# Performance work log

Hardware: AMD Instinct MI355X
Metric: run time of the kernel (lower is better)

Reference implementation:

```python
import jax, jax.numpy as jnp
import numpy as np

N_NODES = 100000
HIDDEN = 64
IN_CH = 128
N_EDGES = 1600000


def setup_inputs() -> dict:
    key = jax.random.key(0)
    ks = jax.random.split(key, 12)
    x = jax.random.normal(ks[0], (N_NODES, IN_CH), dtype=jnp.float32)
    edge_index = jax.random.randint(ks[1], (2, N_EDGES), 0, N_NODES, dtype=jnp.int64)

    def glorot(k, fan_in, fan_out):
        s = jnp.sqrt(6.0 / (fan_in + fan_out)).astype(jnp.float32)
        return jax.random.uniform(k, (fan_in, fan_out), jnp.float32, -s, s)

    return {
        "x": x,
        "edge_index": edge_index,
        # GCNConv layer 1: linear (no bias) + post-aggregation bias
        "W1": glorot(ks[2], IN_CH, HIDDEN),
        "b1": jnp.zeros((HIDDEN,), jnp.float32),
        # GCNConv layer 2
        "W2": glorot(ks[3], HIDDEN, HIDDEN),
        "b2": jnp.zeros((HIDDEN,), jnp.float32),
        # edge classifier MLP: Linear(2H,H) -> ReLU -> Linear(H,2)
        "Wc1": glorot(ks[4], 2 * HIDDEN, HIDDEN),
        "bc1": jnp.zeros((HIDDEN,), jnp.float32),
        "Wc2": glorot(ks[5], HIDDEN, 2),
        "bc2": jnp.zeros((2,), jnp.float32),
    }


def _gcn_forward(x, edge_index, W1, b1, W2, b2, Wc1, bc1, Wc2, bc2):
    n = x.shape[0]
    src, dst = edge_index[0], edge_index[1]
    # add self-loops (PyG GCNConv default)
    loop = jnp.arange(n, dtype=edge_index.dtype)
    a_src = jnp.concatenate([src, loop])  # [E+N]
    a_dst = jnp.concatenate([dst, loop])
    # symmetric normalization: deg over destination with unit edge weights
    deg = jax.ops.segment_sum(jnp.ones(a_dst.shape[0], x.dtype), a_dst, num_segments=n)
    dis = jax.lax.rsqrt(deg)  # deg >= 1 due to self-loops
    norm = dis[a_src] * dis[a_dst]  # [E+N]

    def conv(h, W, b):
        h = h @ W  # [N, H]
        msg = h[a_src] * norm[:, None]  # [E+N, H] gather + scale
        return jax.ops.segment_sum(msg, a_dst, num_segments=n) + b

    h = jax.nn.relu(conv(x, W1, b1))  # dropout is identity in eval mode
    h = conv(h, W2, b2)
    # edge classifier on concatenated endpoint embeddings
    e = jnp.concatenate([h[src], h[dst]], axis=1)  # [E, 2H]
    z = jax.nn.relu(e @ Wc1 + bc1)
    return z @ Wc2 + bc2  # [E, 2]


def reference(x, edge_index, W1, b1, W2, b2, Wc1, bc1, Wc2, bc2):
    return _gcn_forward(x, edge_index, W1, b1, W2, b2, Wc1, bc1, Wc2, bc2)
```

## Files before the change

### kernel.cpp

```cpp
#include <hip/hip_runtime.h>
#include <hip/hip_fp16.h>

#define HID 64

typedef _Float16 half8 __attribute__((ext_vector_type(8)));
typedef _Float16 half4 __attribute__((ext_vector_type(4)));
typedef float f32x4 __attribute__((ext_vector_type(4)));

__global__ void k_count_rank(const int* __restrict__ dst, int* __restrict__ deg,
                             int* __restrict__ rank, int E) {
  int e = blockIdx.x * blockDim.x + threadIdx.x;
  if (e < E) rank[e] = atomicAdd(&deg[dst[e]], 1);
}

__global__ void k_scan1(const int* __restrict__ deg, int* __restrict__ scanout,
                        int* __restrict__ blocksums, float* __restrict__ dis, int n) {
  __shared__ int sdata[256];
  int tid = threadIdx.x;
  int base = blockIdx.x * 1024 + tid * 4;
  int v0 = 0, v1 = 0, v2 = 0, v3 = 0;
  if (base + 0 < n) v0 = deg[base + 0];
  if (base + 1 < n) v1 = deg[base + 1];
  if (base + 2 < n) v2 = deg[base + 2];
  if (base + 3 < n) v3 = deg[base + 3];
  if (base + 0 < n) dis[base + 0] = rsqrtf((float)v0 + 1.0f);
  if (base + 1 < n) dis[base + 1] = rsqrtf((float)v1 + 1.0f);
  if (base + 2 < n) dis[base + 2] = rsqrtf((float)v2 + 1.0f);
  if (base + 3 < n) dis[base + 3] = rsqrtf((float)v3 + 1.0f);
  int tsum = v0 + v1 + v2 + v3;
  sdata[tid] = tsum;
  __syncthreads();
  for (int off = 1; off < 256; off <<= 1) {
    int t = (tid >= off) ? sdata[tid - off] : 0;
    __syncthreads();
    sdata[tid] += t;
    __syncthreads();
  }
  int excl = sdata[tid] - tsum;
  if (base + 0 < n) scanout[base + 0] = excl;
  if (base + 1 < n) scanout[base + 1] = excl + v0;
  if (base + 2 < n) scanout[base + 2] = excl + v0 + v1;
  if (base + 3 < n) scanout[base + 3] = excl + v0 + v1 + v2;
  if (tid == 255) blocksums[blockIdx.x] = sdata[255];
}

__global__ void k_scan2(int* blocksums, int nb) {
  __shared__ int s[128];
  int tid = threadIdx.x;
  int v = (tid < nb) ? blocksums[tid] : 0;
  s[tid] = v;
  __syncthreads();
  for (int off = 1; off < 128; off <<= 1) {
    int t = (tid >= off) ? s[tid - off] : 0;
    __syncthreads();
    s[tid] += t;
    __syncthreads();
  }
  if (tid < nb) blocksums[tid] = s[tid] - v;
}

__global__ void k_scan3(const int* __restrict__ scanout,
                        const int* __restrict__ blocksums, int* __restrict__ rowoff,
                        int n) {
  int i = blockIdx.x * blockDim.x + threadIdx.x;
  if (i < n) rowoff[i] = scanout[i] + blocksums[i >> 10];
}

__global__ void k_scatter_det(const int* __restrict__ src, const int* __restrict__ dst,
                              const int* __restrict__ rowoff,
                              const int* __restrict__ rank,
                              int* __restrict__ csr_src, int E) {
  int e = blockIdx.x * blockDim.x + threadIdx.x;
  if (e >= E) return;
  int pos = rowoff[dst[e]] + rank[e];
  csr_src[pos] = src[e];
}

__global__ void k_pack_all(const float* __restrict__ W1, const float* __restrict__ W2,
                           const float* __restrict__ Wc1, const float* __restrict__ bc1,
                           __half* __restrict__ packW1, __half* __restrict__ packW2,
                           __half* __restrict__ packUV, float* __restrict__ biasUV,
                           __half* __restrict__ ysent) {
  int b = blockIdx.x, tid = threadIdx.x;
  if (b < 4) {
    int t = b * 256 + tid;
    int f = t >> 6, L = t & 63;
    int kc = f >> 2, nb = f & 3;
    int k = 32 * kc + ((L >> 4) << 3);
    int n = (L & 15) + 16 * nb;
    for (int j = 0; j < 8; ++j)
      packW1[(t << 3) + j] = __float2half(W1[(k + j) * 64 + n]);
  } else if (b < 6) {
    int t = (b - 4) * 256 + tid;
    int f = t >> 6, L = t & 63;
    int kc = f >> 2, nb = f & 3;
    int k = 32 * kc + ((L >> 4) << 3);
    int n = (L & 15) + 16 * nb;
    for (int j = 0; j < 8; ++j)
      packW2[(t << 3) + j] = __float2half(W2[(k + j) * 64 + n]);
  } else if (b < 10) {
    int t = (b - 6) * 256 + tid;
    int f = t >> 6, L = t & 63;
    int kc = f >> 3, nb = f & 7;
    int k = 32 * kc + ((L >> 4) << 3);
    int n = (L & 15) + 16 * nb;
    for (int j = 0; j < 8; ++j) {
      float w = (n < 64) ? Wc1[(k + j) * 64 + n] : Wc1[(64 + k + j) * 64 + (n - 64)];
      packUV[(t << 3) + j] = __float2half(w);
    }
  } else {
    if (tid < 128) biasUV[tid] = (tid < 64) ? bc1[tid] : 0.f;
    else if (tid < 192) ysent[tid - 128] = __float2half(0.f);
  }
}

template <int K, int NOUT, bool F32IN>
__global__ __launch_bounds__(256) void k_lin_mfma(
    const void* __restrict__ Xv, const __half* __restrict__ packB,
    const float* __restrict__ bias, const float* __restrict__ dis,
    __half* __restrict__ Y, int n) {
  int wid = blockIdx.x * 4 + (threadIdx.x >> 6);
  int rowbase = wid * 16;
  if (rowbase >= n) return;
  int L = threadIdx.x & 63;
  int m16 = L & 15, quad = L >> 4;
  constexpr int KC = K / 32;
  constexpr int NB = NOUT / 16;

  half8 Bf[KC * NB];
  const half8* packv = (const half8*)packB;
#pragma unroll
  for (int f = 0; f < KC * NB; ++f) Bf[f] = packv[f * 64 + L];

  int r = min(rowbase + m16, n - 1);
  half8 Af[KC];
  if (F32IN) {
    const float* xr = (const float*)Xv + (long)r * K;
#pragma unroll
    for (int kc = 0; kc < KC; ++kc) {
      const float4* xp = (const float4*)(xr + kc * 32 + quad * 8);
      float4 a = xp[0], b = xp[1];
      half8 v = {(_Float16)a.x, (_Float16)a.y, (_Float16)a.z, (_Float16)a.w,
                 (_Float16)b.x, (_Float16)b.y, (_Float16)b.z, (_Float16)b.w};
      Af[kc] = v;
    }
  } else {
    const half8* xr = (const half8*)((const __half*)Xv + (long)r * K);
#pragma unroll
    for (int kc = 0; kc < KC; ++kc) Af[kc] = xr[kc * 4 + quad];
  }

  f32x4 acc[NB];
#pragma unroll
  for (int nb = 0; nb < NB; ++nb) acc[nb] = {0.f, 0.f, 0.f, 0.f};
#pragma unroll
  for (int kc = 0; kc < KC; ++kc)
#pragma unroll
    for (int nb = 0; nb < NB; ++nb)
      acc[nb] = __builtin_amdgcn_mfma_f32_16x16x32_f16(Af[kc], Bf[kc * NB + nb],
                                                       acc[nb], 0, 0, 0);

  float dv[4];
#pragma unroll
  for (int j = 0; j < 4; ++j) {
    int ro = rowbase + quad * 4 + j;
    dv[j] = (dis && ro < n) ? dis[ro] : 1.f;
  }
#pragma unroll
  for (int nb = 0; nb < NB; ++nb) {
    int col = m16 + 16 * nb;
    float bv = bias ? bias[col] : 0.f;
#pragma unroll
    for (int j = 0; j < 4; ++j) {
      int ro = rowbase + quad * 4 + j;
      if (ro < n) {
        float v = (acc[nb][j] + bv) * dv[j];
        Y[(long)ro * NOUT + col] = __float2half(v);
      }
    }
  }
}

__global__ __launch_bounds__(256) void k_agg_csr(
    const __half* __restrict__ Yh, const float* __restrict__ dis,
    const int* __restrict__ rowoff, const int* __restrict__ csr_src,
    const float* __restrict__ b, __half* __restrict__ A, int n, int E, int relu) {
  int node = blockIdx.x * 4 + (threadIdx.x >> 6);
  if (node >= n) return;
  int L = threadIdx.x & 63;
  int sub = L >> 4;
  int cq = L & 15;
  const half4* Y4 = (const half4*)Yh;
  float dd = dis[node];
  int i0 = rowoff[node];
  int end = (node == n - 1) ? E : rowoff[node + 1];

  float z[4][4] = {{0.f}};
  if (sub == 0) {
    half4 hv = Y4[(long)node * 16 + cq];
#pragma unroll
    for (int j = 0; j < 4; ++j) z[0][j] = (float)hv[j];
  }

  int last = end - 1;
  for (int base = i0; base < end; base += 16) {
    int sidx[4];
#pragma unroll
    for (int slot = 0; slot < 4; ++slot) {
      int idx = base + slot * 4 + sub;
      int sl = csr_src[min(idx, last)];
      sidx[slot] = (idx < end) ? sl : n;
    }
#pragma unroll
    for (int slot = 0; slot < 4; ++slot) {
      half4 hv = Y4[(long)sidx[slot] * 16 + cq];
#pragma unroll
      for (int j = 0; j < 4; ++j) z[slot][j] += (float)hv[j];
    }
  }

  float a[4];
#pragma unroll
  for (int j = 0; j < 4; ++j) {
    a[j] = (z[0][j] + z[1][j]) + (z[2][j] + z[3][j]);
    a[j] += __shfl_xor(a[j], 16, 64);
    a[j] += __shfl_xor(a[j], 32, 64);
  }
  if (sub == 0) {
    float4 bb = ((const float4*)b)[cq];
    float v0 = fmaf(a[0], dd, bb.x), v1 = fmaf(a[1], dd, bb.y);
    float v2 = fmaf(a[2], dd, bb.z), v3 = fmaf(a[3], dd, bb.w);
    if (relu) {
      v0 = fmaxf(v0, 0.f); v1 = fmaxf(v1, 0.f);
      v2 = fmaxf(v2, 0.f); v3 = fmaxf(v3, 0.f);
    }
    half4 o = {(_Float16)v0, (_Float16)v1, (_Float16)v2, (_Float16)v3};
    ((half4*)A)[(long)node * 16 + cq] = o;
  }
}

__global__ __launch_bounds__(256) void k_edge_mlp(
    const __half* __restrict__ UV, const int* __restrict__ src,
    const int* __restrict__ dst, const float* __restrict__ Wc2,
    const float* __restrict__ bc2, float* __restrict__ out, int E, int nwaves) {
  int wid = blockIdx.x * 4 + (threadIdx.x >> 6);
  int L = threadIdx.x & 63;
  int sub = L >> 4;
  int cq = L & 15;

  float w0[4], w1[4];
#pragma unroll
  for (int j = 0; j < 4; ++j) {
    int c = cq * 4 + j;
    w0[j] = Wc2[2 * c];
    w1[j] = Wc2[2 * c + 1];
  }
  float ob0 = bc2[0], ob1 = bc2[1];

  const half4* UV4 = (const half4*)UV;
  int last = E - 1;

  for (long base = (long)wid * 32; base < E; base += (long)nwaves * 32) {
    int se[8], de[8];
#pragma unroll
    for (int slot = 0; slot < 8; ++slot) {
      int e = (int)base + slot * 4 + sub;
      int ec = min(e, last);
      se[slot] = src[ec];
      de[slot] = dst[ec];
    }
    half4 uu[8], vv[8];
#pragma unroll
    for (int slot = 0; slot < 8; ++slot) {
      uu[slot] = UV4[(long)se[slot] * 32 + cq];
      vv[slot] = UV4[(long)de[slot] * 32 + 16 + cq];
    }
#pragma unroll
    for (int slot = 0; slot < 8; ++slot) {
      float o0 = 0.f, o1 = 0.f;
#pragma unroll
      for (int j = 0; j < 4; ++j) {
        float v = fmaxf((float)uu[slot][j] + (float)vv[slot][j], 0.f);
        o0 = fmaf(v, w0[j], o0);
        o1 = fmaf(v, w1[j], o1);
      }
      o0 += __shfl_xor(o0, 1, 64);
      o1 += __shfl_xor(o1, 1, 64);
      o0 += __shfl_xor(o0, 2, 64);
      o1 += __shfl_xor(o1, 2, 64);
      o0 += __shfl_xor(o0, 4, 64);
      o1 += __shfl_xor(o1, 4, 64);
      o0 += __shfl_xor(o0, 8, 64);
      o1 += __shfl_xor(o1, 8, 64);
      int e = (int)base + slot * 4 + sub;
      if (cq == 0 && e < E) {
        float2 o = {o0 + ob0, o1 + ob1};
        *(float2*)(out + 2 * (long)e) = o;
      }
    }
  }
}

extern "C" void kernel_launch(void* const* d_in, const int* in_sizes, int n_in,
                              void* d_out, int out_size, void* d_ws, size_t ws_size,
                              hipStream_t stream) {
  const float* x   = (const float*)d_in[0];
  const int*   ei  = (const int*)d_in[1];
  const float* W1  = (const float*)d_in[2];
  const float* b1  = (const float*)d_in[3];
  const float* W2  = (const float*)d_in[4];
  const float* b2  = (const float*)d_in[5];
  const float* Wc1 = (const float*)d_in[6];
  const float* bc1 = (const float*)d_in[7];
  const float* Wc2 = (const float*)d_in[8];
  const float* bc2 = (const float*)d_in[9];

  const int N = in_sizes[0] / 128;
  const int E = in_sizes[1] / 2;
  const int* src = ei;
  const int* dst = ei + E;

  float* dis     = (float*)d_ws;
  __half* y      = (__half*)(dis + N);
  __half* h      = y + (long)(N + 1) * HID;
  __half* UV     = h + (long)N * HID;
  __half* packW1 = UV + (long)N * 128;
  __half* packW2 = packW1 + 8192;
  __half* packUV = packW2 + 4096;
  float* biasUV  = (float*)(packUV + 8192);
  int* degi      = (int*)(biasUV + 128);
  int* scanout   = degi + N;
  int* rowoff    = scanout + N;
  int* blocksums = rowoff + N;
  int* csr_src   = blocksums + 128;
  int* rank      = (int*)y;

  const int B = 256;
  int gN  = (N + B - 1) / B;
  int gE  = (E + B - 1) / B;
  int nb  = (N + 1023) / 1024;
  int gLin = (N + 63) / 64;

  hipMemsetAsync(degi, 0, (size_t)N * sizeof(int), stream);
  k_pack_all<<<11, B, 0, stream>>>(W1, W2, Wc1, bc1, packW1, packW2, packUV,
                                   biasUV, y + (long)N * HID);
  k_count_rank<<<gE, B, 0, stream>>>(dst, degi, rank, E);
  k_scan1<<<nb, B, 0, stream>>>(degi, scanout, blocksums, dis, N);
  k_scan2<<<1, 128, 0, stream>>>(blocksums, nb);
  k_scan3<<<gN, B, 0, stream>>>(scanout, blocksums, rowoff, N);
  k_scatter_det<<<gE, B, 0, stream>>>(src, dst, rowoff, rank, csr_src, E);

  int gAgg = (N + 3) / 4;

  k_lin_mfma<128, 64, true><<<gLin, B, 0, stream>>>(x, packW1, nullptr, dis, y, N);
  k_agg_csr<<<gAgg, B, 0, stream>>>(y, dis, rowoff, csr_src, b1, h, N, E, 1);

  k_lin_mfma<64, 64, false><<<gLin, B, 0, stream>>>(h, packW2, nullptr, dis, y, N);
  k_agg_csr<<<gAgg, B, 0, stream>>>(y, dis, rowoff, csr_src, b2, h, N, E, 0);

  k_lin_mfma<64, 128, false><<<gLin, B, 0, stream>>>(h, packUV, biasUV, nullptr, UV, N);
  int cblocks = 2048;
  int nwaves = cblocks * 4;
  k_edge_mlp<<<cblocks, B, 0, stream>>>(UV, src, dst, Wc2, bc2,
                                        (float*)d_out, E, nwaves);
}
```

Measured before the change: 388.0 us.

## Build CSR with two-level bucketed counting sort instead of global atomics

Replaces the global-atomic degree count, rank, and scatter with a two-pass bucket sort. Edges are first partitioned into 1024-node buckets using per-chunk shared-memory histograms and a scan. Each bucket is then sorted locally in LDS to produce row offsets, dis, and csr_src. This targets the contended global atomics and random scatter across the whole node range, at the cost of extra kernels and an intermediate psrc/pdst buffer. Within-row edge order now depends on LDS atomic order rather than the previous global rank.

```diff
diff --git a/kernel.cpp b/kernel.cpp
--- a/kernel.cpp
+++ b/kernel.cpp
@@ -2,31 +2,37 @@
 #include <hip/hip_fp16.h>
 
 #define HID 64
+#define BKT_SHIFT 10
+#define BKT_NODES 1024
+#define PCHUNKS 512
 
 typedef _Float16 half8 __attribute__((ext_vector_type(8)));
 typedef _Float16 half4 __attribute__((ext_vector_type(4)));
 typedef float f32x4 __attribute__((ext_vector_type(4)));
 
-__global__ void k_count_rank(const int* __restrict__ dst, int* __restrict__ deg,
-                             int* __restrict__ rank, int E) {
-  int e = blockIdx.x * blockDim.x + threadIdx.x;
-  if (e < E) rank[e] = atomicAdd(&deg[dst[e]], 1);
-}
-
-__global__ void k_scan1(const int* __restrict__ deg, int* __restrict__ scanout,
-                        int* __restrict__ blocksums, float* __restrict__ dis, int n) {
+__global__ __launch_bounds__(256) void k_bkt_count(const int* __restrict__ dst,
+                                                   int* __restrict__ G, int E,
+                                                   int nbkt, int chunk) {
+  __shared__ int hist[128];
+  int p = blockIdx.x, tid = threadIdx.x;
+  for (int i = tid; i < nbkt; i += 256) hist[i] = 0;
+  __syncthreads();
+  int s = p * chunk, e = min(s + chunk, E);
+  for (int i = s + tid; i < e; i += 256) atomicAdd(&hist[dst[i] >> BKT_SHIFT], 1);
+  __syncthreads();
+  for (int b = tid; b < nbkt; b += 256) G[b * PCHUNKS + p] = hist[b];
+}
+
+__global__ void k_scan1(const int* __restrict__ in, int* __restrict__ scanout,
+                        int* __restrict__ blocksums, int n) {
   __shared__ int sdata[256];
   int tid = threadIdx.x;
   int base = blockIdx.x * 1024 + tid * 4;
   int v0 = 0, v1 = 0, v2 = 0, v3 = 0;
-  if (base + 0 < n) v0 = deg[base + 0];
-  if (base + 1 < n) v1 = deg[base + 1];
-  if (base + 2 < n) v2 = deg[base + 2];
-  if (base + 3 < n) v3 = deg[base + 3];
-  if (base + 0 < n) dis[base + 0] = rsqrtf((float)v0 + 1.0f);
-  if (base + 1 < n) dis[base + 1] = rsqrtf((float)v1 + 1.0f);
-  if (base + 2 < n) dis[base + 2] = rsqrtf((float)v2 + 1.0f);
-  if (base + 3 < n) dis[base + 3] = rsqrtf((float)v3 + 1.0f);
+  if (base + 0 < n) v0 = in[base + 0];
+  if (base + 1 < n) v1 = in[base + 1];
+  if (base + 2 < n) v2 = in[base + 2];
+  if (base + 3 < n) v3 = in[base + 3];
   int tsum = v0 + v1 + v2 + v3;
   sdata[tid] = tsum;
   __syncthreads();
@@ -60,20 +66,72 @@
 }
 
 __global__ void k_scan3(const int* __restrict__ scanout,
-                        const int* __restrict__ blocksums, int* __restrict__ rowoff,
+                        const int* __restrict__ blocksums, int* __restrict__ outp,
                         int n) {
   int i = blockIdx.x * blockDim.x + threadIdx.x;
-  if (i < n) rowoff[i] = scanout[i] + blocksums[i >> 10];
-}
-
-__global__ void k_scatter_det(const int* __restrict__ src, const int* __restrict__ dst,
-                              const int* __restrict__ rowoff,
-                              const int* __restrict__ rank,
-                              int* __restrict__ csr_src, int E) {
-  int e = blockIdx.x * blockDim.x + threadIdx.x;
-  if (e >= E) return;
-  int pos = rowoff[dst[e]] + rank[e];
-  csr_src[pos] = src[e];
+  if (i < n) outp[i] = scanout[i] + blocksums[i >> 10];
+}
+
+__global__ __launch_bounds__(256) void k_bkt_scatter(
+    const int* __restrict__ src, const int* __restrict__ dst,
+    const int* __restrict__ Gscan, int* __restrict__ psrc,
+    unsigned short* __restrict__ pdst, int E, int nbkt, int chunk) {
+  __shared__ int gbase[128];
+  __shared__ int rcnt[128];
+  int p = blockIdx.x, tid = threadIdx.x;
+  for (int b = tid; b < nbkt; b += 256) {
+    gbase[b] = Gscan[b * PCHUNKS + p];
+    rcnt[b] = 0;
+  }
+  __syncthreads();
+  int s = p * chunk, e = min(s + chunk, E);
+  for (int i = s + tid; i < e; i += 256) {
+    int d = dst[i];
+    int b = d >> BKT_SHIFT;
+    int r = atomicAdd(&rcnt[b], 1);
+    int pos = gbase[b] + r;
+    psrc[pos] = src[i];
+    pdst[pos] = (unsigned short)(d & (BKT_NODES - 1));
+  }
+}
+
+__global__ __launch_bounds__(1024) void k_bkt_final(
+    const int* __restrict__ Gscan, const int* __restrict__ psrc,
+    const unsigned short* __restrict__ pdst, int* __restrict__ rowoff,
+    float* __restrict__ dis, int* __restrict__ csr_src, int E, int nbkt, int N) {
+  __shared__ int cnt[BKT_NODES];
+  __shared__ int lo[BKT_NODES];
+  int b = blockIdx.x, tid = threadIdx.x;
+  int s = Gscan[b * PCHUNKS];
+  int eend = (b + 1 < nbkt) ? Gscan[(b + 1) * PCHUNKS] : E;
+  cnt[tid] = 0;
+  __syncthreads();
+  for (int i = s + tid; i < eend; i += 1024) atomicAdd(&cnt[pdst[i]], 1);
+  __syncthreads();
+  int v = cnt[tid];
+  lo[tid] = v;
+  __syncthreads();
+  for (int off = 1; off < 1024; off <<= 1) {
+    int t = (tid >= off) ? lo[tid - off] : 0;
+    __syncthreads();
+    lo[tid] += t;
+    __syncthreads();
+  }
+  int excl = lo[tid] - v;
+  int node = b * BKT_NODES + tid;
+  if (node < N) {
+    rowoff[node] = s + excl;
+    dis[node] = rsqrtf((float)v + 1.0f);
+  }
+  __syncthreads();
+  lo[tid] = excl;
+  cnt[tid] = 0;
+  __syncthreads();
+  for (int i = s + tid; i < eend; i += 1024) {
+    int ln = pdst[i];
+    int r = atomicAdd(&cnt[ln], 1);
+    csr_src[s + lo[ln] + r] = psrc[i];
+  }
 }
 
 __global__ void k_pack_all(const float* __restrict__ W1, const float* __restrict__ W2,
@@ -320,6 +378,10 @@
   const int* src = ei;
   const int* dst = ei + E;
 
+  const int nbkt = (N + BKT_NODES - 1) >> BKT_SHIFT;
+  const int gsz = nbkt * PCHUNKS;
+  const int chunk = (E + PCHUNKS - 1) / PCHUNKS;
+
   float* dis     = (float*)d_ws;
   __half* y      = (__half*)(dis + N);
   __half* h      = y + (long)(N + 1) * HID;
@@ -328,29 +390,31 @@
   __half* packW2 = packW1 + 8192;
   __half* packUV = packW2 + 4096;
   float* biasUV  = (float*)(packUV + 8192);
-  int* degi      = (int*)(biasUV + 128);
-  int* scanout   = degi + N;
-  int* rowoff    = scanout + N;
-  int* blocksums = rowoff + N;
-  int* csr_src   = blocksums + 128;
-  int* rank      = (int*)y;
+  int* rowoff    = (int*)(biasUV + 128);
+  int* csr_src   = rowoff + N;
+  int* G         = csr_src + E;
+  int* Gs1       = G + gsz;
+  int* Gbs       = Gs1 + gsz;
+  int* Gscan     = Gbs + 128;
+  int* psrc            = (int*)UV;
+  unsigned short* pdst = (unsigned short*)(psrc + E);
 
   const int B = 256;
-  int gN  = (N + B - 1) / B;
-  int gE  = (E + B - 1) / B;
-  int nb  = (N + 1023) / 1024;
-  int gLin = (N + 63) / 64;
-
-  hipMemsetAsync(degi, 0, (size_t)N * sizeof(int), stream);
+  int nbScan = (gsz + 1023) / 1024;
+
   k_pack_all<<<11, B, 0, stream>>>(W1, W2, Wc1, bc1, packW1, packW2, packUV,
                                    biasUV, y + (long)N * HID);
-  k_count_rank<<<gE, B, 0, stream>>>(dst, degi, rank, E);
-  k_scan1<<<nb, B, 0, stream>>>(degi, scanout, blocksums, dis, N);
-  k_scan2<<<1, 128, 0, stream>>>(blocksums, nb);
-  k_scan3<<<gN, B, 0, stream>>>(scanout, blocksums, rowoff, N);
-  k_scatter_det<<<gE, B, 0, stream>>>(src, dst, rowoff, rank, csr_src, E);
+  k_bkt_count<<<PCHUNKS, B, 0, stream>>>(dst, G, E, nbkt, chunk);
+  k_scan1<<<nbScan, B, 0, stream>>>(G, Gs1, Gbs, gsz);
+  k_scan2<<<1, 128, 0, stream>>>(Gbs, nbScan);
+  k_scan3<<<(gsz + B - 1) / B, B, 0, stream>>>(Gs1, Gbs, Gscan, gsz);
+  k_bkt_scatter<<<PCHUNKS, B, 0, stream>>>(src, dst, Gscan, psrc, pdst, E, nbkt,
+                                           chunk);
+  k_bkt_final<<<nbkt, 1024, 0, stream>>>(Gscan, psrc, pdst, rowoff, dis, csr_src,
+                                         E, nbkt, N);
 
   int gAgg = (N + 3) / 4;
+  int gLin = (N + 63) / 64;
 
   k_lin_mfma<128, 64, true><<<gLin, B, 0, stream>>>(x, packW1, nullptr, dis, y, N);
   k_agg_csr<<<gAgg, B, 0, stream>>>(y, dis, rowoff, csr_src, b1, h, N, E, 1);
```

Result: faster. 343.0 us (-11.6%).
